# Kernel tuning notes

Measured on AMD Instinct MI355X. Metric: run time of the kernel, lower is better.

## Reference

```python
import jax, jax.numpy as jnp
import numpy as np

N = 100000      # nodes
E = 1600000     # edges (avg degree 16)
F = 128         # feature dim (in == out)
H = 4           # heads
ALPHA = 0.2     # leaky relu slope


def setup_inputs() -> dict:
    key = jax.random.key(0)
    k1, k2, k3, k4, k5 = jax.random.split(key, 5)
    inputs = jax.random.normal(k1, (N, F), dtype=jnp.float32)
    # ensure every node appears as a destination row (src of message) so rowsum > 0
    src = jnp.concatenate([jnp.arange(N, dtype=jnp.int32),
                           jax.random.randint(k2, (E - N,), 0, N, dtype=jnp.int32)])
    dst = jax.random.randint(k3, (E,), 0, N, dtype=jnp.int32)
    edge = jnp.stack([src, dst])  # [2, E], rows = adj.indices()
    adj_values = jax.random.uniform(k4, (E,), dtype=jnp.float32)
    W = jnp.ones((H, F), dtype=jnp.float32)  # nn.init.ones_ per head
    stdv = 1.0 / np.sqrt(2.0 * F)
    a = jax.random.uniform(k5, (H, 2 * F), dtype=jnp.float32, minval=-stdv, maxval=stdv)
    return {"inputs": inputs, "edge": edge, "adj_values": adj_values, "W": W, "a": a}


def reference(inputs, edge, adj_values, W, a):
    src, dst = edge[0], edge[1]
    acc = jnp.zeros_like(inputs)
    for k in range(H):  # small fixed head loop (distinct params per head)
        h = inputs * W[k]                       # [N, F] elementwise scale
        # a.mm([h_src; h_dst]) decomposes into per-node partial scores
        s_src = h @ a[k, :F]                    # [N]
        s_dst = h @ a[k, F:]                    # [N]
        e = jnp.exp(jax.nn.leaky_relu(s_src[src] + s_dst[dst], ALPHA)) * adj_values  # [E]
        rowsum = jax.ops.segment_sum(e, src, num_segments=N)               # [N]
        h_prime = jax.ops.segment_sum(e[:, None] * h[dst], src, num_segments=N)  # [N, F]
        acc = acc + jax.nn.elu(h_prime / rowsum[:, None])  # concat=True -> elu
    return acc / H  # mean over heads
```

## Files before the change

### kernel.cpp

```cpp
#include <hip/hip_runtime.h>

#define FDIM   128
#define HEADS  4
#define ALPHA  0.2f
#define DMASK  0x03FFFFFF
#define PT     4096
#define NBMAX  1568

typedef float v2f __attribute__((ext_vector_type(2)));

__device__ __forceinline__ float readlane_f(float v, int lane) {
  return __int_as_float(__builtin_amdgcn_readlane(__float_as_int(v), lane));
}

__global__ __launch_bounds__(256) void score_kernel(
    const float* __restrict__ x, const float* __restrict__ W,
    const float* __restrict__ a, float* __restrict__ s_src,
    float* __restrict__ s_dst, unsigned int* __restrict__ xb,
    const int* __restrict__ src, int* __restrict__ hist,
    int E, int HB, int n) {
  __shared__ int h[NBMAX];
  int lane = threadIdx.x & 63;
  int node = (blockIdx.x << 2) + (threadIdx.x >> 6);
  if (node < n) {
    const float2* x2 = (const float2*)x;
    const float2* W2 = (const float2*)W;
    const float2* a2 = (const float2*)a;
    float2 xv = x2[(size_t)node * 64 + lane];

    unsigned int u0 = __float_as_uint(xv.x);
    unsigned int u1 = __float_as_uint(xv.y);
    u0 += 0x7fffu + ((u0 >> 16) & 1u);
    u1 += 0x7fffu + ((u1 >> 16) & 1u);
    xb[(size_t)node * 64 + lane] = (u0 >> 16) | (u1 & 0xffff0000u);

#pragma unroll
    for (int k = 0; k < HEADS; k++) {
      float2 wv = W2[k * 64 + lane];
      float hx = xv.x * wv.x, hy = xv.y * wv.y;
      float2 as_ = a2[k * 128 + lane];
      float2 ad_ = a2[k * 128 + 64 + lane];
      float rs = hx * as_.x + hy * as_.y;
      float rd = hx * ad_.x + hy * ad_.y;
#pragma unroll
      for (int off = 32; off > 0; off >>= 1) {
        rs += __shfl_down(rs, off);
        rd += __shfl_down(rd, off);
      }
      if (lane == 0) {
        s_src[node * HEADS + k] = rs;
        s_dst[node * HEADS + k] = rd;
      }
    }
  }

  int b = blockIdx.x;
  if (b < HB) {
    int t = threadIdx.x;
    int NB = (n + 63) >> 6;
    for (int i = t; i < NB; i += 256) h[i] = 0;
    __syncthreads();
    int base = b * 8192;
#pragma unroll 4
    for (int j = 0; j < 32; j++) {
      int i = base + j * 256 + t;
      if (i < E) atomicAdd(&h[src[i] >> 6], 1);
    }
    __syncthreads();
    for (int i = t; i < NB; i += 256)
      if (h[i]) atomicAdd(&hist[i], h[i]);
  }
}

__global__ __launch_bounds__(256) void scan_kernel(const int* __restrict__ hist,
                                                   int* __restrict__ fine_ptr,
                                                   int* __restrict__ cursor,
                                                   int NB, int E) {
  __shared__ int lds[256];
  int t = threadIdx.x;
  int loc[8];
  int s = 0;
#pragma unroll
  for (int j = 0; j < 8; j++) {
    int idx = t * 8 + j;
    loc[j] = (idx < NB) ? hist[idx] : 0;
    s += loc[j];
  }
  lds[t] = s;
  __syncthreads();
  for (int off = 1; off < 256; off <<= 1) {
    int xv = (t >= off) ? lds[t - off] : 0;
    __syncthreads();
    lds[t] += xv;
    __syncthreads();
  }
  int run = lds[t] - s;
#pragma unroll
  for (int j = 0; j < 8; j++) {
    int idx = t * 8 + j;
    if (idx < NB) {
      fine_ptr[idx] = run;
      cursor[idx]   = run;
    }
    run += loc[j];
  }
  if (t == 0) fine_ptr[NB] = E;
}

__global__ __launch_bounds__(256) void partition_kernel(
    const int* __restrict__ src, const int* __restrict__ dst,
    const float* __restrict__ adj, int* __restrict__ cursor,
    int2* __restrict__ ebuf, int E, int NB) {
  __shared__ int h[NBMAX];
  __shared__ int sc[NBMAX];
  __shared__ int bg[NBMAX];
  __shared__ unsigned short keyarr[PT];
  __shared__ int2 es[PT];
  __shared__ int lds[256];

  int t = threadIdx.x;
  int base = blockIdx.x * PT;
  for (int i = t; i < NB; i += 256) h[i] = 0;
  __syncthreads();

  int ssrc[16];
#pragma unroll
  for (int j = 0; j < 16; j++) {
    int i = base + j * 256 + t;
    ssrc[j] = (i < E) ? src[i] : -1;
    if (ssrc[j] >= 0) atomicAdd(&h[ssrc[j] >> 6], 1);
  }
  __syncthreads();

  int loc[8];
  int s = 0;
#pragma unroll
  for (int j = 0; j < 8; j++) {
    int idx = t * 8 + j;
    loc[j] = (idx < NB) ? h[idx] : 0;
    s += loc[j];
  }
  lds[t] = s;
  __syncthreads();
  for (int off = 1; off < 256; off <<= 1) {
    int xv = (t >= off) ? lds[t - off] : 0;
    __syncthreads();
    lds[t] += xv;
    __syncthreads();
  }
  int run = lds[t] - s;
#pragma unroll
  for (int j = 0; j < 8; j++) {
    int idx = t * 8 + j;
    if (idx < NB) sc[idx] = run;
    run += loc[j];
  }
  __syncthreads();

  for (int i = t; i < NB; i += 256)
    if (h[i]) bg[i] = atomicAdd(&cursor[i], h[i]);
  __syncthreads();

#pragma unroll
  for (int j = 0; j < 16; j++) {
    if (ssrc[j] >= 0) {
      int i = base + j * 256 + t;
      int k = ssrc[j] >> 6;
      int slot = atomicAdd(&sc[k], 1);
      int2 pk;
      pk.x = (int)(((unsigned)(ssrc[j] & 63) << 26) | (unsigned)dst[i]);
      pk.y = __float_as_int(adj[i]);
      es[slot] = pk;
      keyarr[slot] = (unsigned short)k;
    }
  }
  __syncthreads();

  int tc = E - base; if (tc > PT) tc = PT;
  for (int s2 = t; s2 < tc; s2 += 256) {
    int k = keyarr[s2];
    int rank = s2 - (sc[k] - h[k]);
    ebuf[bg[k] + rank] = es[s2];
  }
}

__global__ __launch_bounds__(256, 4) void aggregate_kernel(
    const unsigned int* __restrict__ xb, const float* __restrict__ W,
    const float* __restrict__ s_src, const float* __restrict__ s_dst,
    const int* __restrict__ fine_ptr, const int2* __restrict__ ebuf,
    float* __restrict__ out, int n) {
  __shared__ int2  es[2048];
  __shared__ float evbuf[4][64];
  __shared__ int   nbeg[65];
  __shared__ int   nrun[64];
  __shared__ int   h[64];

  int t = threadIdx.x, b = blockIdx.x;
  int lane = t & 63, wid = t >> 6;
  int beg = fine_ptr[b];
  int L   = fine_ptr[b + 1] - beg;

  if (t < 64) h[t] = 0;
  __syncthreads();
  for (int i = t; i < L; i += 256)
    atomicAdd(&h[(unsigned)ebuf[beg + i].x >> 26], 1);
  __syncthreads();
  if (t < 64) {
    int v = h[t];
#pragma unroll
    for (int off = 1; off < 64; off <<= 1) {
      int u = __shfl_up(v, off);
      if (lane >= off) v += u;
    }
    nbeg[t + 1] = v;
    nrun[t] = v - h[t];
    if (t == 0) nbeg[0] = 0;
  }
  __syncthreads();
  for (int i = t; i < L; i += 256) {
    int2 pk = ebuf[beg + i];
    int kk = (unsigned)pk.x >> 26;
    int slot = atomicAdd(&nrun[kk], 1);
    es[slot] = pk;
  }
  __syncthreads();

  int e = lane >> 2;
  int k = lane & 3;

  for (int ni = 0; ni < 16; ni++) {
    int nl = wid * 16 + ni;
    int node = (b << 6) + nl;
    if (node >= n) break;
    int eb = nbeg[nl], cnt = nbeg[nl + 1] - eb;
    float ssrc_k = s_src[node * HEADS + k];

    v2f acc0{0.f,0.f}, acc1{0.f,0.f}, acc2{0.f,0.f}, acc3{0.f,0.f};
    float rsum = 0.f;

    int c = 0;
    while (c < cnt) {
      int cn = cnt - c; if (cn > 16) cn = 16;
      int2 pk{0, 0};
      if (e < cn) pk = es[eb + c + e];
      int dv = pk.x & DMASK;

      float sdv = s_dst[dv * HEADS + k];
      int dd[16];
#pragma unroll
      for (int j = 0; j < 16; j++)
        dd[j] = __builtin_amdgcn_readlane(pk.x, j * 4) & DMASK;
      unsigned int xw[16];
#pragma unroll
      for (int j = 0; j < 16; j++)
        xw[j] = xb[((unsigned)dd[j] << 6) + lane];

      float s = ssrc_k + sdv;
      s = (s >= 0.f) ? s : ALPHA * s;
      float ev = __expf(s) * __int_as_float(pk.y);
      rsum += ev;
      evbuf[wid][lane] = ev;

#pragma unroll
      for (int j = 0; j < 16; j++) {
        const float4 s4 = *(const float4*)&evbuf[wid][j * 4];
        v2f xv;
        xv.x = __uint_as_float(xw[j] << 16);
        xv.y = __uint_as_float(xw[j] & 0xffff0000u);
        acc0 += s4.x * xv;
        acc1 += s4.y * xv;
        acc2 += s4.z * xv;
        acc3 += s4.w * xv;
      }
      c += 16;
    }

    rsum += __shfl_xor(rsum, 4);
    rsum += __shfl_xor(rsum, 8);
    rsum += __shfl_xor(rsum, 16);
    rsum += __shfl_xor(rsum, 32);
    float r0 = readlane_f(rsum, 0), r1 = readlane_f(rsum, 1);
    float r2 = readlane_f(rsum, 2), r3 = readlane_f(rsum, 3);

    const float2* W2 = (const float2*)W;
    float2 o{0.f, 0.f};
    float hx, hy;
    {
      float2 wv = W2[0 * 64 + lane];
      hx = wv.x * acc0.x / r0; hy = wv.y * acc0.y / r0;
      o.x += (hx > 0.f) ? hx : expm1f(hx); o.y += (hy > 0.f) ? hy : expm1f(hy);
    }
    {
      float2 wv = W2[1 * 64 + lane];
      hx = wv.x * acc1.x / r1; hy = wv.y * acc1.y / r1;
      o.x += (hx > 0.f) ? hx : expm1f(hx); o.y += (hy > 0.f) ? hy : expm1f(hy);
    }
    {
      float2 wv = W2[2 * 64 + lane];
      hx = wv.x * acc2.x / r2; hy = wv.y * acc2.y / r2;
      o.x += (hx > 0.f) ? hx : expm1f(hx); o.y += (hy > 0.f) ? hy : expm1f(hy);
    }
    {
      float2 wv = W2[3 * 64 + lane];
      hx = wv.x * acc3.x / r3; hy = wv.y * acc3.y / r3;
      o.x += (hx > 0.f) ? hx : expm1f(hx); o.y += (hy > 0.f) ? hy : expm1f(hy);
    }
    o.x *= 0.25f; o.y *= 0.25f;
    ((float2*)out)[(size_t)node * 64 + lane] = o;
  }
}

extern "C" void kernel_launch(void* const* d_in, const int* in_sizes, int n_in,
                              void* d_out, int out_size, void* d_ws, size_t ws_size,
                              hipStream_t stream) {
  const float* x   = (const float*)d_in[0];
  const int*   edg = (const int*)d_in[1];
  const float* adj = (const float*)d_in[2];
  const float* W   = (const float*)d_in[3];
  const float* a   = (const float*)d_in[4];
  float* out = (float*)d_out;

  int E = in_sizes[2];
  int n = in_sizes[0] / FDIM;
  const int* src = edg;
  const int* dst = edg + E;
  int NB = (n + 63) >> 6;
  int HB = (E + 8191) / 8192;

  auto align = [](size_t v) { return (v + 255) & ~(size_t)255; };
  char* ws = (char*)d_ws;
  int*   fine_ptr = (int*)ws;          ws += align((size_t)(NB + 1) * 4);
  int*   cursor   = (int*)ws;          ws += align((size_t)NB * 4);
  int*   hist     = (int*)ws;          ws += align((size_t)NB * 4);
  int2*  ebuf     = (int2*)ws;         ws += align((size_t)E * 8);
  float* s_src    = (float*)ws;        ws += align((size_t)n * HEADS * 4);
  float* s_dst    = (float*)ws;        ws += align((size_t)n * HEADS * 4);
  unsigned int* xb = (unsigned int*)ws; ws += align((size_t)n * 64 * 4);

  hipMemsetAsync(hist, 0, (size_t)NB * 4, stream);

  score_kernel<<<(n + 3) / 4, 256, 0, stream>>>(x, W, a, s_src, s_dst, xb,
                                                src, hist, E, HB, n);
  scan_kernel<<<1, 256, 0, stream>>>(hist, fine_ptr, cursor, NB, E);
  partition_kernel<<<(E + PT - 1) / PT, 256, 0, stream>>>(src, dst, adj, cursor,
                                                          ebuf, E, NB);
  aggregate_kernel<<<NB, 256, 0, stream>>>(xb, W, s_src, s_dst, fine_ptr,
                                           ebuf, out, n);
}
```

Measured before the change: 321.6 us.

## Split aggregate blocks in half and use fast reciprocal/exp in epilogue

Each 64-node bucket now goes to two blocks that each handle 32 nodes. Every block filters the bucket's edges by the top bit of the local node index, so the LDS edge stage shrinks to 1024 entries and the launch bound rises to allow 8 blocks per CU, aiming at more parallelism and better latency hiding. The epilogue computes one reciprocal of the row sum and multiplies by it instead of dividing, and replaces expm1f with __expf(x)-1. In exchange, each block reads the whole bucket's edge list twice, and the ELU and normalisation are slightly less accurate near zero.

New measurement: 282.2 us. -12.2%, faster.

```diff
diff --git a/kernel.cpp b/kernel.cpp
--- a/kernel.cpp
+++ b/kernel.cpp
@@ -184,31 +184,34 @@
   }
 }
 
-__global__ __launch_bounds__(256, 4) void aggregate_kernel(
+__global__ __launch_bounds__(256, 8) void aggregate_kernel(
     const unsigned int* __restrict__ xb, const float* __restrict__ W,
     const float* __restrict__ s_src, const float* __restrict__ s_dst,
     const int* __restrict__ fine_ptr, const int2* __restrict__ ebuf,
     float* __restrict__ out, int n) {
-  __shared__ int2  es[2048];
+  __shared__ int2  es[1024];
   __shared__ float evbuf[4][64];
-  __shared__ int   nbeg[65];
-  __shared__ int   nrun[64];
-  __shared__ int   h[64];
-
-  int t = threadIdx.x, b = blockIdx.x;
+  __shared__ int   nbeg[33];
+  __shared__ int   nrun[32];
+  __shared__ int   h[32];
+
+  int t = threadIdx.x, bb = blockIdx.x;
+  int b0 = bb >> 1, half = bb & 1;
   int lane = t & 63, wid = t >> 6;
-  int beg = fine_ptr[b];
-  int L   = fine_ptr[b + 1] - beg;
-
-  if (t < 64) h[t] = 0;
-  __syncthreads();
-  for (int i = t; i < L; i += 256)
-    atomicAdd(&h[(unsigned)ebuf[beg + i].x >> 26], 1);
-  __syncthreads();
-  if (t < 64) {
+  int beg = fine_ptr[b0];
+  int L   = fine_ptr[b0 + 1] - beg;
+
+  if (t < 32) h[t] = 0;
+  __syncthreads();
+  for (int i = t; i < L; i += 256) {
+    int kk = (unsigned)ebuf[beg + i].x >> 26;
+    if ((kk >> 5) == half) atomicAdd(&h[kk & 31], 1);
+  }
+  __syncthreads();
+  if (t < 32) {
     int v = h[t];
 #pragma unroll
-    for (int off = 1; off < 64; off <<= 1) {
+    for (int off = 1; off < 32; off <<= 1) {
       int u = __shfl_up(v, off);
       if (lane >= off) v += u;
     }
@@ -220,17 +223,19 @@
   for (int i = t; i < L; i += 256) {
     int2 pk = ebuf[beg + i];
     int kk = (unsigned)pk.x >> 26;
-    int slot = atomicAdd(&nrun[kk], 1);
-    es[slot] = pk;
+    if ((kk >> 5) == half) {
+      int slot = atomicAdd(&nrun[kk & 31], 1);
+      es[slot] = pk;
+    }
   }
   __syncthreads();
 
   int e = lane >> 2;
   int k = lane & 3;
 
-  for (int ni = 0; ni < 16; ni++) {
-    int nl = wid * 16 + ni;
-    int node = (b << 6) + nl;
+  for (int ni = 0; ni < 8; ni++) {
+    int nl = wid * 8 + ni;
+    int node = (b0 << 6) + (half << 5) + nl;
     if (node >= n) break;
     int eb = nbeg[nl], cnt = nbeg[nl + 1] - eb;
     float ssrc_k = s_src[node * HEADS + k];
@@ -279,31 +284,36 @@
     rsum += __shfl_xor(rsum, 8);
     rsum += __shfl_xor(rsum, 16);
     rsum += __shfl_xor(rsum, 32);
-    float r0 = readlane_f(rsum, 0), r1 = readlane_f(rsum, 1);
-    float r2 = readlane_f(rsum, 2), r3 = readlane_f(rsum, 3);
+    float rinv = __builtin_amdgcn_rcpf(rsum);
+    float r0 = readlane_f(rinv, 0), r1 = readlane_f(rinv, 1);
+    float r2 = readlane_f(rinv, 2), r3 = readlane_f(rinv, 3);
 
     const float2* W2 = (const float2*)W;
     float2 o{0.f, 0.f};
     float hx, hy;
     {
       float2 wv = W2[0 * 64 + lane];
-      hx = wv.x * acc0.x / r0; hy = wv.y * acc0.y / r0;
-      o.x += (hx > 0.f) ? hx : expm1f(hx); o.y += (hy > 0.f) ? hy : expm1f(hy);
+      hx = wv.x * acc0.x * r0; hy = wv.y * acc0.y * r0;
+      o.x += (hx > 0.f) ? hx : (__expf(hx) - 1.f);
+      o.y += (hy > 0.f) ? hy : (__expf(hy) - 1.f);
     }
     {
       float2 wv = W2[1 * 64 + lane];
-      hx = wv.x * acc1.x / r1; hy = wv.y * acc1.y / r1;
-      o.x += (hx > 0.f) ? hx : expm1f(hx); o.y += (hy > 0.f) ? hy : expm1f(hy);
+      hx = wv.x * acc1.x * r1; hy = wv.y * acc1.y * r1;
+      o.x += (hx > 0.f) ? hx : (__expf(hx) - 1.f);
+      o.y += (hy > 0.f) ? hy : (__expf(hy) - 1.f);
     }
     {
       float2 wv = W2[2 * 64 + lane];
-      hx = wv.x * acc2.x / r2; hy = wv.y * acc2.y / r2;
-      o.x += (hx > 0.f) ? hx : expm1f(hx); o.y += (hy > 0.f) ? hy : expm1f(hy);
+      hx = wv.x * acc2.x * r2; hy = wv.y * acc2.y * r2;
+      o.x += (hx > 0.f) ? hx : (__expf(hx) - 1.f);
+      o.y += (hy > 0.f) ? hy : (__expf(hy) - 1.f);
     }
     {
       float2 wv = W2[3 * 64 + lane];
-      hx = wv.x * acc3.x / r3; hy = wv.y * acc3.y / r3;
-      o.x += (hx > 0.f) ? hx : expm1f(hx); o.y += (hy > 0.f) ? hy : expm1f(hy);
+      hx = wv.x * acc3.x * r3; hy = wv.y * acc3.y * r3;
+      o.x += (hx > 0.f) ? hx : (__expf(hx) - 1.f);
+      o.y += (hy > 0.f) ? hy : (__expf(hy) - 1.f);
     }
     o.x *= 0.25f; o.y *= 0.25f;
     ((float2*)out)[(size_t)node * 64 + lane] = o;
@@ -344,6 +354,6 @@
   scan_kernel<<<1, 256, 0, stream>>>(hist, fine_ptr, cursor, NB, E);
   partition_kernel<<<(E + PT - 1) / PT, 256, 0, stream>>>(src, dst, adj, cursor,
                                                           ebuf, E, NB);
-  aggregate_kernel<<<NB, 256, 0, stream>>>(xb, W, s_src, s_dst, fine_ptr,
-                                           ebuf, out, n);
-}
+  aggregate_kernel<<<NB * 2, 256, 0, stream>>>(xb, W, s_src, s_dst, fine_ptr,
+                                               ebuf, out, n);
+}
```
